# Kernel tuning notes

Measured on AMD Instinct MI355X. Metric: run time of the kernel, lower is better.

## Reference

```python
import jax, jax.numpy as jnp
from jax import lax
import numpy as np

B, C, H, W = 1, 128, 32, 32
OC, K = 128, 3
STRIDE, PAD, DIL = 1, 1, 1
ARRAY_SIZE = 32
QUANT = 8


def setup_inputs() -> dict:
    key = jax.random.key(0)
    k1, k2, k3 = jax.random.split(key, 3)
    x = jax.random.normal(k1, (B, C, H, W), dtype=jnp.float32)
    weight = jax.random.normal(k2, (OC, C, K, K), dtype=jnp.float32) * 0.05
    bias = jax.random.normal(k3, (OC,), dtype=jnp.float32) * 0.05
    return {"x": x, "weight": weight, "bias": bias}


def _conv(x, w, b):
    out = lax.conv_general_dilated(
        x, w, window_strides=(STRIDE, STRIDE),
        padding=((PAD, PAD), (PAD, PAD)),
        rhs_dilation=(DIL, DIL),
        dimension_numbers=("NCHW", "OIHW", "NCHW"))
    return out + b[None, :, None, None]


def _unfold(x, oh, ow):
    # torch F.unfold: (B, C*K*K, L) with channel-major ordering (c, kh, kw)
    xp = jnp.pad(x, ((0, 0), (0, 0), (PAD, PAD), (PAD, PAD)))
    cols = jnp.stack(
        [xp[:, :, i:i + oh, j:j + ow] for i in range(K) for j in range(K)],
        axis=2)  # (B, C, K*K, OH, OW)
    return cols.reshape(B, C * K * K, oh * ow)


def reference(x, weight, bias):
    oh = (H + 2 * PAD - DIL * (K - 1) - 1) // STRIDE + 1
    ow = (W + 2 * PAD - DIL * (K - 1) - 1) // STRIDE + 1
    L = oh * ow
    qmax = float(2 ** QUANT - 1)

    # --- set_quant_params: per-spatial-location scale/zero_point from full conv out ---
    out_full = _conv(x, weight, bias).reshape(1, OC, -1)  # (1, OC, L)
    mx = jnp.max(out_full, axis=1)  # (1, L)
    mn = jnp.min(out_full, axis=1)
    scale = (mx - mn) / qmax
    zp = jnp.clip(-mn / scale, 0.0, qmax)
    zp = jnp.where(jnp.isnan(zp), 0.0, zp)
    zp = jnp.trunc(zp)  # .int() truncation
    scale = lax.stop_gradient(scale)[:, None, None, :]  # (1,1,1,L)
    zp = lax.stop_gradient(zp)[:, None, None, :]

    # --- unfold + explicit elementwise multiply (crossbar expansion) ---
    cols = _unfold(x, oh, ow)                       # (B, C*K*K, L)
    pre = cols[:, None, :, :] * weight.reshape(1, OC, C * K * K, 1)  # (B,OC,CKK,L)

    # pad front of dim 2 to a multiple of array_size (pads a full chunk if divisible)
    ckk = C * K * K
    pad_d3 = ARRAY_SIZE - ckk % ARRAY_SIZE
    pre = jnp.pad(pre, ((0, 0), (0, 0), (pad_d3, 0), (0, 0)))

    # block-sum over array_size chunks (crossbar partial sums)
    n_chunks = (ckk + pad_d3) // ARRAY_SIZE
    accu = pre.reshape(B, OC, n_chunks, ARRAY_SIZE, L).sum(axis=3)  # (B,OC,n_chunks,L)

    # per-chunk fake-quant (Quant8F) with straight-through estimator
    q = jnp.clip(jnp.round(accu / scale) + zp, 0.0, qmax)
    deq = (q - zp) * scale
    quant_accu = accu + lax.stop_gradient(deq - accu)

    # reduce over chunks -> conv output (note: bias is NOT added in original forward)
    return quant_accu.sum(axis=2).reshape(B, OC, oh, ow)
```

## Files before the change

kernel.cpp:

```cpp
#include <hip/hip_runtime.h>

#define L_    1024
#define CKK_  1152
#define QMAX_ 255.0f
#define NCH   36

__global__ __launch_bounds__(256) void wtrans(
    const float* __restrict__ w, float* __restrict__ wt)
{
    const int e  = blockIdx.x * 256 + threadIdx.x;
    const int oc = e / 288, tq = e - 288 * oc;
    const float4 v = ((const float4*)(w + oc * CKK_))[tq];
    ((float4*)wt)[tq * 128 + oc] = v;
}

template <bool WT>
__global__ __launch_bounds__(512) void fused_cas(
    const float* __restrict__ x,
    const float* __restrict__ w,
    const float4* __restrict__ wt4,
    const float* __restrict__ bias,
    float* __restrict__ out)
{
    __shared__ __align__(16) float  xs[NCH * 32 * 4];
    __shared__ __align__(16) float4 vbuf[NCH][128];
    __shared__ float red[8][4];
    __shared__ float spar[2][2][3];
    __shared__ float qb[4][128];

    const int t   = threadIdx.x;
    const int b   = blockIdx.x;
    const int oc  = t & 127;
    const int g   = t >> 7;
    const int ppe = g & 1;
    const int oh  = b >> 3;
    const int ow0 = (b & 7) * 4;
    const int l0  = b * 4;

    for (int i = 0; i < 9; ++i) {
        const int e   = i * 512 + t;
        const int j   = e >> 7;
        const int tap = (e >> 2) & 31;
        const int px  = e & 3;
        const int d   = j * 32 + tap;
        const int c   = d / 9, r = d - 9 * c;
        const int kh  = r / 3, kw = r - 3 * kh;
        const int iy  = oh + kh - 1, ix = ow0 + px + kw - 1;
        const bool ok = ((unsigned)iy < 32u) & ((unsigned)ix < 32u);
        const float vv = x[ok ? (c * 1024 + iy * 32 + ix) : 0];
        xs[e] = ok ? vv : 0.f;
    }
    __syncthreads();

    const float4* wrow = (const float4*)(w + oc * CKK_);

    auto load8 = [&](float4* dst, int j) {
#pragma unroll
        for (int k4 = 0; k4 < 8; ++k4)
            dst[k4] = WT ? wt4[(j * 8 + k4) * 128 + oc] : wrow[j * 8 + k4];
    };

    auto chunk = [&](int j, const float4* wreg) {
        float a0 = 0.f, a1 = 0.f, a2 = 0.f, a3 = 0.f;
        const float4* xj = (const float4*)(xs + j * 128);
#pragma unroll
        for (int k4 = 0; k4 < 8; ++k4) {
            const float4 wv = wreg[k4];
            const float4 x0 = xj[4 * k4 + 0];
            const float4 x1 = xj[4 * k4 + 1];
            const float4 x2 = xj[4 * k4 + 2];
            const float4 x3 = xj[4 * k4 + 3];
            a0 = fmaf(wv.x, x0.x, a0); a1 = fmaf(wv.x, x0.y, a1);
            a2 = fmaf(wv.x, x0.z, a2); a3 = fmaf(wv.x, x0.w, a3);
            a0 = fmaf(wv.y, x1.x, a0); a1 = fmaf(wv.y, x1.y, a1);
            a2 = fmaf(wv.y, x1.z, a2); a3 = fmaf(wv.y, x1.w, a3);
            a0 = fmaf(wv.z, x2.x, a0); a1 = fmaf(wv.z, x2.y, a1);
            a2 = fmaf(wv.z, x2.z, a2); a3 = fmaf(wv.z, x2.w, a3);
            a0 = fmaf(wv.w, x3.x, a0); a1 = fmaf(wv.w, x3.y, a1);
            a2 = fmaf(wv.w, x3.z, a2); a3 = fmaf(wv.w, x3.w, a3);
        }
        vbuf[j][oc] = make_float4(a0, a1, a2, a3);
    };

    {
        const int jb = g * 9;
        float4 wc[8], wn[8];
        load8(wc, jb);
#pragma unroll
        for (int jj = 0; jj < 8; jj += 2) {
            const int j0 = jb + jj;
            load8(wn, j0 + 1);
            chunk(j0, wc);
            load8(wc, j0 + 2);
            chunk(j0 + 1, wn);
        }
        chunk(jb + 8, wc);
    }
    __syncthreads();

    float s0 = 0.f, s1 = 0.f;
    for (int j = 0; j < NCH; ++j) {
        const float4 vv = vbuf[j][oc];
        s0 += (ppe == 0) ? vv.x : vv.z;
        s1 += (ppe == 0) ? vv.y : vv.w;
    }
    const float bval = bias[oc];
    const float t0 = s0 + bval, t1 = s1 + bval;

    float mn0 = t0, mx0 = t0, mn1 = t1, mx1 = t1;
#pragma unroll
    for (int off = 32; off > 0; off >>= 1) {
        mn0 = fminf(mn0, __shfl_xor(mn0, off));
        mx0 = fmaxf(mx0, __shfl_xor(mx0, off));
        mn1 = fminf(mn1, __shfl_xor(mn1, off));
        mx1 = fmaxf(mx1, __shfl_xor(mx1, off));
    }
    const int wv = t >> 6;
    if ((t & 63) == 0) {
        red[wv][0] = mn0; red[wv][1] = mx0;
        red[wv][2] = mn1; red[wv][3] = mx1;
    }
    __syncthreads();
    if ((t & 63) == 0 && (wv & 1) == 0 && wv < 4) {
        const int pw = wv ^ 1;
        const float amn0 = fminf(mn0, red[pw][0]);
        const float amx0 = fmaxf(mx0, red[pw][1]);
        const float amn1 = fminf(mn1, red[pw][2]);
        const float amx1 = fmaxf(mx1, red[pw][3]);
        {
            const float sv = (amx0 - amn0) / QMAX_;
            float z = -amn0 / sv;
            z = fmaxf(z, 0.f);
            z = fminf(z, QMAX_);
            z = truncf(z);
            spar[ppe][0][0] = sv; spar[ppe][0][1] = z; spar[ppe][0][2] = 1.0f / sv;
        }
        {
            const float sv = (amx1 - amn1) / QMAX_;
            float z = -amn1 / sv;
            z = fmaxf(z, 0.f);
            z = fminf(z, QMAX_);
            z = truncf(z);
            spar[ppe][1][0] = sv; spar[ppe][1][1] = z; spar[ppe][1][2] = 1.0f / sv;
        }
    }
    __syncthreads();

    const float sc0 = spar[ppe][0][0], zp0 = spar[ppe][0][1], iv0 = spar[ppe][0][2];
    const float sc1 = spar[ppe][1][0], zp1 = spar[ppe][1][1], iv1 = spar[ppe][1][2];
    float q0 = 0.f, q1 = 0.f;
    for (int j = 0; j < NCH; ++j) {
        const float4 vv = vbuf[j][oc];
        const float v0 = (ppe == 0) ? vv.x : vv.z;
        const float v1 = (ppe == 0) ? vv.y : vv.w;
        float qn0 = rintf(v0 * iv0) + zp0;
        qn0 = fminf(fmaxf(qn0, 0.f), QMAX_);
        q0 += (qn0 - zp0) * sc0;
        float qn1 = rintf(v1 * iv1) + zp1;
        qn1 = fminf(fmaxf(qn1, 0.f), QMAX_);
        q1 += (qn1 - zp1) * sc1;
    }
    if (t < 256) {
        qb[2 * ppe + 0][oc] = q0;
        qb[2 * ppe + 1][oc] = q1;
    }
    __syncthreads();

    if (t < 128)
        *(float4*)(out + (size_t)t * L_ + l0) =
            make_float4(qb[0][t], qb[1][t], qb[2][t], qb[3][t]);
}

extern "C" void kernel_launch(void* const* d_in, const int* in_sizes, int n_in,
                              void* d_out, int out_size, void* d_ws, size_t ws_size,
                              hipStream_t stream) {
    const float* x    = (const float*)d_in[0];
    const float* w    = (const float*)d_in[1];
    const float* bias = (const float*)d_in[2];
    float* out = (float*)d_out;
    float* ws  = (float*)d_ws;

    const size_t wt_need = (size_t)288 * 128 * 16;
    if (ws_size >= wt_need) {
        wtrans<<<144, 256, 0, stream>>>((const float*)d_in[1], ws);
        fused_cas<true><<<256, 512, 0, stream>>>(
            x, w, (const float4*)ws, bias, out);
    } else {
        fused_cas<false><<<256, 512, 0, stream>>>(
            x, w, nullptr, bias, out);
    }
}
```

Baseline: 69.48 us.

## Prebuild im2col buffer in global memory and read it with uniform loads

```diff
diff --git a/kernel.cpp b/kernel.cpp
--- a/kernel.cpp
+++ b/kernel.cpp
@@ -14,31 +14,16 @@
     ((float4*)wt)[tq * 128 + oc] = v;
 }
 
-template <bool WT>
-__global__ __launch_bounds__(512) void fused_cas(
-    const float* __restrict__ x,
-    const float* __restrict__ w,
-    const float4* __restrict__ wt4,
-    const float* __restrict__ bias,
-    float* __restrict__ out)
+__global__ __launch_bounds__(256) void xcol_build(
+    const float* __restrict__ x, float* __restrict__ xcol)
 {
-    __shared__ __align__(16) float  xs[NCH * 32 * 4];
-    __shared__ __align__(16) float4 vbuf[NCH][128];
-    __shared__ float red[8][4];
-    __shared__ float spar[2][2][3];
-    __shared__ float qb[4][128];
-
+    const int b   = blockIdx.x;
     const int t   = threadIdx.x;
-    const int b   = blockIdx.x;
-    const int oc  = t & 127;
-    const int g   = t >> 7;
-    const int ppe = g & 1;
     const int oh  = b >> 3;
     const int ow0 = (b & 7) * 4;
-    const int l0  = b * 4;
-
-    for (int i = 0; i < 9; ++i) {
-        const int e   = i * 512 + t;
+    float* dst = xcol + b * 4608;
+    for (int i = 0; i < 18; ++i) {
+        const int e   = i * 256 + t;
         const int j   = e >> 7;
         const int tap = (e >> 2) & 31;
         const int px  = e & 3;
@@ -48,28 +33,72 @@
         const int iy  = oh + kh - 1, ix = ow0 + px + kw - 1;
         const bool ok = ((unsigned)iy < 32u) & ((unsigned)ix < 32u);
         const float vv = x[ok ? (c * 1024 + iy * 32 + ix) : 0];
-        xs[e] = ok ? vv : 0.f;
-    }
-    __syncthreads();
+        dst[e] = ok ? vv : 0.f;
+    }
+}
+
+template <bool FAST>
+__global__ __launch_bounds__(512) void fused_cas(
+    const float* __restrict__ x,
+    const float* __restrict__ w,
+    const float4* __restrict__ wt4,
+    const float* __restrict__ xcol,
+    const float* __restrict__ bias,
+    float* __restrict__ out)
+{
+    __shared__ __align__(16) float4 vbuf[NCH][128];
+    __shared__ __align__(16) float  xs[NCH * 32 * 4];
+    __shared__ float red[8][4];
+    __shared__ float spar[2][2][3];
+    __shared__ float qb[4][128];
+
+    const int t   = threadIdx.x;
+    const int b   = blockIdx.x;
+    const int oc  = t & 127;
+    const int g   = t >> 7;
+    const int ppe = g & 1;
+    const int oh  = b >> 3;
+    const int ow0 = (b & 7) * 4;
+    const int l0  = b * 4;
+
+    if constexpr (!FAST) {
+        for (int i = 0; i < 9; ++i) {
+            const int e   = i * 512 + t;
+            const int j   = e >> 7;
+            const int tap = (e >> 2) & 31;
+            const int px  = e & 3;
+            const int d   = j * 32 + tap;
+            const int c   = d / 9, r = d - 9 * c;
+            const int kh  = r / 3, kw = r - 3 * kh;
+            const int iy  = oh + kh - 1, ix = ow0 + px + kw - 1;
+            const bool ok = ((unsigned)iy < 32u) & ((unsigned)ix < 32u);
+            const float vv = x[ok ? (c * 1024 + iy * 32 + ix) : 0];
+            xs[e] = ok ? vv : 0.f;
+        }
+        __syncthreads();
+    }
+
+    const float* xb = FAST
+        ? (xcol + __builtin_amdgcn_readfirstlane(b * 4608)) : nullptr;
 
     const float4* wrow = (const float4*)(w + oc * CKK_);
 
     auto load8 = [&](float4* dst, int j) {
 #pragma unroll
         for (int k4 = 0; k4 < 8; ++k4)
-            dst[k4] = WT ? wt4[(j * 8 + k4) * 128 + oc] : wrow[j * 8 + k4];
+            dst[k4] = FAST ? wt4[(j * 8 + k4) * 128 + oc] : wrow[j * 8 + k4];
     };
 
     auto chunk = [&](int j, const float4* wreg) {
         float a0 = 0.f, a1 = 0.f, a2 = 0.f, a3 = 0.f;
-        const float4* xj = (const float4*)(xs + j * 128);
+        const float* xj = FAST ? (xb + j * 128) : (xs + j * 128);
 #pragma unroll
         for (int k4 = 0; k4 < 8; ++k4) {
             const float4 wv = wreg[k4];
-            const float4 x0 = xj[4 * k4 + 0];
-            const float4 x1 = xj[4 * k4 + 1];
-            const float4 x2 = xj[4 * k4 + 2];
-            const float4 x3 = xj[4 * k4 + 3];
+            const float4 x0 = *(const float4*)(xj + (4 * k4 + 0) * 4);
+            const float4 x1 = *(const float4*)(xj + (4 * k4 + 1) * 4);
+            const float4 x2 = *(const float4*)(xj + (4 * k4 + 2) * 4);
+            const float4 x3 = *(const float4*)(xj + (4 * k4 + 3) * 4);
             a0 = fmaf(wv.x, x0.x, a0); a1 = fmaf(wv.x, x0.y, a1);
             a2 = fmaf(wv.x, x0.z, a2); a3 = fmaf(wv.x, x0.w, a3);
             a0 = fmaf(wv.y, x1.x, a0); a1 = fmaf(wv.y, x1.y, a1);
@@ -180,13 +209,18 @@
     float* out = (float*)d_out;
     float* ws  = (float*)d_ws;
 
-    const size_t wt_need = (size_t)288 * 128 * 16;
-    if (ws_size >= wt_need) {
-        wtrans<<<144, 256, 0, stream>>>((const float*)d_in[1], ws);
+    const size_t wt_floats = (size_t)288 * 128 * 4;
+    const size_t xc_floats = (size_t)256 * 4608;
+    const size_t need = (wt_floats + xc_floats) * 4;
+    if (ws_size >= need) {
+        float* wt = ws;
+        float* xc = ws + wt_floats;
+        wtrans<<<144, 256, 0, stream>>>(w, wt);
+        xcol_build<<<256, 256, 0, stream>>>(x, xc);
         fused_cas<true><<<256, 512, 0, stream>>>(
-            x, w, (const float4*)ws, bias, out);
+            x, w, (const float4*)wt, xc, bias, out);
     } else {
         fused_cas<false><<<256, 512, 0, stream>>>(
-            x, w, nullptr, bias, out);
-    }
-}
+            x, w, nullptr, nullptr, bias, out);
+    }
+}
```

After: 89.36 us. 1.29x slower.

## Compute two output channels per thread with uneven chunk split across waves

Applied to the files above, without the earlier changes.

```diff
diff --git a/kernel.cpp b/kernel.cpp
--- a/kernel.cpp
+++ b/kernel.cpp
@@ -28,14 +28,16 @@
     __shared__ float spar[2][2][3];
     __shared__ float qb[4][128];
 
-    const int t   = threadIdx.x;
-    const int b   = blockIdx.x;
-    const int oc  = t & 127;
-    const int g   = t >> 7;
-    const int ppe = g & 1;
-    const int oh  = b >> 3;
-    const int ow0 = (b & 7) * 4;
-    const int l0  = b * 4;
+    const int t    = threadIdx.x;
+    const int b    = blockIdx.x;
+    const int lane = t & 63;
+    const int g    = t >> 6;
+    const int oc0  = 2 * lane;
+    const int oc   = t & 127;
+    const int ppe  = (t >> 7) & 1;
+    const int oh   = b >> 3;
+    const int ow0  = (b & 7) * 4;
+    const int l0   = b * 4;
 
     for (int i = 0; i < 9; ++i) {
         const int e   = i * 512 + t;
@@ -52,49 +54,62 @@
     }
     __syncthreads();
 
-    const float4* wrow = (const float4*)(w + oc * CKK_);
-
-    auto load8 = [&](float4* dst, int j) {
+    const bool five = (g < 4);
+    const int  jb   = five ? (5 * g) : (4 * g + 4);
+
+    const float4* wrow0 = (const float4*)(w + (oc0 + 0) * CKK_);
+    const float4* wrow1 = (const float4*)(w + (oc0 + 1) * CKK_);
+
+    auto load16 = [&](float4* dst, int j) {
 #pragma unroll
-        for (int k4 = 0; k4 < 8; ++k4)
-            dst[k4] = WT ? wt4[(j * 8 + k4) * 128 + oc] : wrow[j * 8 + k4];
+        for (int k4 = 0; k4 < 8; ++k4) {
+            dst[2 * k4 + 0] = WT ? wt4[(j * 8 + k4) * 128 + oc0]     : wrow0[j * 8 + k4];
+            dst[2 * k4 + 1] = WT ? wt4[(j * 8 + k4) * 128 + oc0 + 1] : wrow1[j * 8 + k4];
+        }
     };
 
-    auto chunk = [&](int j, const float4* wreg) {
+    auto chunk2 = [&](int j, const float4* wreg) {
         float a0 = 0.f, a1 = 0.f, a2 = 0.f, a3 = 0.f;
+        float a4 = 0.f, a5 = 0.f, a6 = 0.f, a7 = 0.f;
         const float4* xj = (const float4*)(xs + j * 128);
 #pragma unroll
         for (int k4 = 0; k4 < 8; ++k4) {
-            const float4 wv = wreg[k4];
+            const float4 w0 = wreg[2 * k4 + 0];
+            const float4 w1 = wreg[2 * k4 + 1];
             const float4 x0 = xj[4 * k4 + 0];
             const float4 x1 = xj[4 * k4 + 1];
             const float4 x2 = xj[4 * k4 + 2];
             const float4 x3 = xj[4 * k4 + 3];
-            a0 = fmaf(wv.x, x0.x, a0); a1 = fmaf(wv.x, x0.y, a1);
-            a2 = fmaf(wv.x, x0.z, a2); a3 = fmaf(wv.x, x0.w, a3);
-            a0 = fmaf(wv.y, x1.x, a0); a1 = fmaf(wv.y, x1.y, a1);
-            a2 = fmaf(wv.y, x1.z, a2); a3 = fmaf(wv.y, x1.w, a3);
-            a0 = fmaf(wv.z, x2.x, a0); a1 = fmaf(wv.z, x2.y, a1);
-            a2 = fmaf(wv.z, x2.z, a2); a3 = fmaf(wv.z, x2.w, a3);
-            a0 = fmaf(wv.w, x3.x, a0); a1 = fmaf(wv.w, x3.y, a1);
-            a2 = fmaf(wv.w, x3.z, a2); a3 = fmaf(wv.w, x3.w, a3);
-        }
-        vbuf[j][oc] = make_float4(a0, a1, a2, a3);
+            a0 = fmaf(w0.x, x0.x, a0); a1 = fmaf(w0.x, x0.y, a1);
+            a2 = fmaf(w0.x, x0.z, a2); a3 = fmaf(w0.x, x0.w, a3);
+            a0 = fmaf(w0.y, x1.x, a0); a1 = fmaf(w0.y, x1.y, a1);
+            a2 = fmaf(w0.y, x1.z, a2); a3 = fmaf(w0.y, x1.w, a3);
+            a0 = fmaf(w0.z, x2.x, a0); a1 = fmaf(w0.z, x2.y, a1);
+            a2 = fmaf(w0.z, x2.z, a2); a3 = fmaf(w0.z, x2.w, a3);
+            a0 = fmaf(w0.w, x3.x, a0); a1 = fmaf(w0.w, x3.y, a1);
+            a2 = fmaf(w0.w, x3.z, a2); a3 = fmaf(w0.w, x3.w, a3);
+            a4 = fmaf(w1.x, x0.x, a4); a5 = fmaf(w1.x, x0.y, a5);
+            a6 = fmaf(w1.x, x0.z, a6); a7 = fmaf(w1.x, x0.w, a7);
+            a4 = fmaf(w1.y, x1.x, a4); a5 = fmaf(w1.y, x1.y, a5);
+            a6 = fmaf(w1.y, x1.z, a6); a7 = fmaf(w1.y, x1.w, a7);
+            a4 = fmaf(w1.z, x2.x, a4); a5 = fmaf(w1.z, x2.y, a5);
+            a6 = fmaf(w1.z, x2.z, a6); a7 = fmaf(w1.z, x2.w, a7);
+            a4 = fmaf(w1.w, x3.x, a4); a5 = fmaf(w1.w, x3.y, a5);
+            a6 = fmaf(w1.w, x3.z, a6); a7 = fmaf(w1.w, x3.w, a7);
+        }
+        vbuf[j][oc0 + 0] = make_float4(a0, a1, a2, a3);
+        vbuf[j][oc0 + 1] = make_float4(a4, a5, a6, a7);
     };
 
     {
-        const int jb = g * 9;
-        float4 wc[8], wn[8];
-        load8(wc, jb);
-#pragma unroll
-        for (int jj = 0; jj < 8; jj += 2) {
-            const int j0 = jb + jj;
-            load8(wn, j0 + 1);
-            chunk(j0, wc);
-            load8(wc, j0 + 2);
-            chunk(j0 + 1, wn);
-        }
-        chunk(jb + 8, wc);
+        float4 wc[16], wn[16];
+        load16(wc, jb + 0);
+        load16(wn, jb + 1);
+        chunk2(jb + 0, wc); load16(wc, jb + 2);
+        chunk2(jb + 1, wn); load16(wn, jb + 3);
+        chunk2(jb + 2, wc); if (five) load16(wc, jb + 4);
+        chunk2(jb + 3, wn);
+        if (five) chunk2(jb + 4, wc);
     }
     __syncthreads();
 
@@ -182,7 +197,7 @@
 
     const size_t wt_need = (size_t)288 * 128 * 16;
     if (ws_size >= wt_need) {
-        wtrans<<<144, 256, 0, stream>>>((const float*)d_in[1], ws);
+        wtrans<<<144, 256, 0, stream>>>(w, ws);
         fused_cas<true><<<256, 512, 0, stream>>>(
             x, w, (const float4*)ws, bias, out);
     } else {
```

New measurement: 71.22 us. +2.5%, slower.
